# Kernel optimization log

Measured on AMD Instinct MI355X. Metric: run time of the kernel, lower is better.

## Reference

```python
import jax, jax.numpy as jnp
import numpy as np

B, N = 4, 2048
VD, CD = 256, 64
H = 4
INNER = VD  # inner_ratio = 1
D = INNER // H  # head_dim = 64
EPS = 1e-5
RMS_EPS = 1e-6


def layer_norm(x, g, b):
    m = jnp.mean(x, axis=-1, keepdims=True)
    v = jnp.mean((x - m) ** 2, axis=-1, keepdims=True)
    return (x - m) * jax.lax.rsqrt(v + EPS) * g + b


def rms_norm(x, s):
    ms = jnp.mean(x * x, axis=-1, keepdims=True)
    return x * jax.lax.rsqrt(ms + RMS_EPS) * s


def split_heads(x):  # (b, n, h*d) -> (b, h, n, d)
    b, n, _ = x.shape
    return x.reshape(b, n, H, D).transpose(0, 2, 1, 3)


def setup_inputs() -> dict:
    key = jax.random.key(0)
    ks = jax.random.split(key, 10)
    w = lambda k, shp: jax.random.normal(k, shp, dtype=jnp.float32) * 0.02
    return {
        "V": jax.random.normal(ks[0], (B, N, VD), dtype=jnp.float32),
        "C": jax.random.normal(ks[1], (B, N, CD), dtype=jnp.float32),
        "vn_g": jnp.ones((VD,), jnp.float32), "vn_b": jnp.zeros((VD,), jnp.float32),
        "cn_g": jnp.ones((CD,), jnp.float32), "cn_b": jnp.zeros((CD,), jnp.float32),
        "W_vqk": w(ks[2], (VD, 2 * INNER)), "b_vqk": jnp.zeros((2 * INNER,), jnp.float32),
        "rms_v": jnp.ones((2 * INNER,), jnp.float32),
        "W_cqk": w(ks[3], (CD, 2 * INNER)), "b_cqk": jnp.zeros((2 * INNER,), jnp.float32),
        "rms_c": jnp.ones((2 * INNER,), jnp.float32),
        "W_vv": w(ks[4], (VD, INNER)), "b_vv": jnp.zeros((INNER,), jnp.float32),
        "W_cv": w(ks[5], (CD, INNER)), "b_cv": jnp.zeros((INNER,), jnp.float32),
        "W_ov": w(ks[6], (INNER, VD)), "b_ov": jnp.zeros((VD,), jnp.float32),
        "W_oc": w(ks[7], (INNER, CD)), "b_oc": jnp.zeros((CD,), jnp.float32),
    }


def reference(V, C, vn_g, vn_b, cn_g, cn_b, W_vqk, b_vqk, rms_v, W_cqk, b_cqk, rms_c,
              W_vv, b_vv, W_cv, b_cv, W_ov, b_ov, W_oc, b_oc):
    Vn = layer_norm(V, vn_g, vn_b)
    Cn = layer_norm(C, cn_g, cn_b)
    qkv = rms_norm(Vn @ W_vqk + b_vqk, rms_v)
    qkc = rms_norm(Cn @ W_cqk + b_cqk, rms_c)
    qv, kv = jnp.split(qkv, 2, axis=-1)
    qc, kc = jnp.split(qkc, 2, axis=-1)
    vv = Vn @ W_vv + b_vv
    vc = Cn @ W_cv + b_cv
    qv, kv, vv, qc, kc, vc = map(split_heads, (qv, kv, vv, qc, kc, vc))
    # shared attention map: softmax((QvKv^T + QcKc^T)/sqrt(d))
    scores = (jnp.einsum("bhnd,bhmd->bhnm", qv, kv)
              + jnp.einsum("bhnd,bhmd->bhnm", qc, kc)) / np.sqrt(D).astype(np.float32)
    attn = jax.nn.softmax(scores, axis=-1)
    out_v = jnp.einsum("bhnm,bhmd->bhnd", attn, vv).transpose(0, 2, 1, 3).reshape(B, N, INNER)
    out_c = jnp.einsum("bhnm,bhmd->bhnd", attn, vc).transpose(0, 2, 1, 3).reshape(B, N, INNER)
    return out_v @ W_ov + b_ov, out_c @ W_oc + b_oc
```

## Files before the change

kernel.cpp:

```cpp
#include <hip/hip_runtime.h>

typedef unsigned short u16;
typedef unsigned int   u32;
typedef short s16x8 __attribute__((ext_vector_type(8)));
typedef float f32x4 __attribute__((ext_vector_type(4)));

#define WS_STATSV 0
#define WS_STATSC 65536
#define WS_WT_VQK 131072
#define WS_WT_CQK 393216
#define WS_WT_VV  458752
#define WS_WT_CV  589824
#define WS_WT_OV  622592
#define WS_WT_OC  753664
#define WS_Q      786432
#define WS_K      9175040
#define WS_VT     17563648
#define WS_OV     25952256
#define WS_OC     30146560

__device__ __forceinline__ float bf2f(u16 h){
  union { u32 u; float f; } x; x.u = ((u32)h) << 16; return x.f;
}
__device__ __forceinline__ u16 f2bf(float f){
  union { float f; u32 u; } x; x.f = f;
  u32 u = x.u; u += 0x7fffu + ((u >> 16) & 1u);
  return (u16)(u >> 16);
}
__device__ __forceinline__ f32x4 mfma16(s16x8 a, s16x8 b, f32x4 c){
  return __builtin_amdgcn_mfma_f32_16x16x32_bf16(a, b, c, 0, 0, 0);
}

__global__ __launch_bounds__(256) void k_prep(const float* V, const float* C,
    const float* vng, const float* vnb, const float* cng, const float* cnb,
    const float* Wvqk, const float* Wcqk, const float* Wvv, const float* Wcv,
    const float* Wov, const float* Woc, char* ws){
  int bid = blockIdx.x;
  if (bid < 4096){
    int wid = threadIdx.x >> 6, lane = threadIdx.x & 63;
    if (bid < 2048){
      int row = bid*4 + wid;
      const float4* p = (const float4*)(V + row*256);
      float4 v = p[lane];
      float s = v.x+v.y+v.z+v.w, s2 = v.x*v.x+v.y*v.y+v.z*v.z+v.w*v.w;
      for (int d=1; d<64; d<<=1){ s += __shfl_xor(s,d); s2 += __shfl_xor(s2,d); }
      float m = s*(1.0f/256.0f); float var = s2*(1.0f/256.0f) - m*m; if (var < 0.f) var = 0.f;
      float rstd = rsqrtf(var + 1e-5f), nb = -m*rstd;
      float4 gg = ((const float4*)vng)[lane];
      float4 bb = ((const float4*)vnb)[lane];
      ushort4 pk;
      pk.x = f2bf(fmaf(fmaf(v.x, rstd, nb), gg.x, bb.x));
      pk.y = f2bf(fmaf(fmaf(v.y, rstd, nb), gg.y, bb.y));
      pk.z = f2bf(fmaf(fmaf(v.z, rstd, nb), gg.z, bb.z));
      pk.w = f2bf(fmaf(fmaf(v.w, rstd, nb), gg.w, bb.w));
      *(ushort4*)((u16*)(ws + WS_OV) + row*256 + lane*4) = pk;
    } else {
      int row = (bid-2048)*4 + wid;
      float x = C[row*64 + lane];
      float s = x, s2 = x*x;
      for (int d=1; d<64; d<<=1){ s += __shfl_xor(s,d); s2 += __shfl_xor(s2,d); }
      float m = s*(1.0f/64.0f); float var = s2*(1.0f/64.0f) - m*m; if (var < 0.f) var = 0.f;
      float rstd = rsqrtf(var + 1e-5f);
      float xn = fmaf(fmaf(x, rstd, -m*rstd), cng[lane], cnb[lane]);
      ((u16*)(ws + WS_OC))[row*64 + lane] = f2bf(xn);
    }
  } else {
    int tb = bid - 4096;
    const float* src; u16* dst; int K, N, rel;
    if      (tb <  64){ src=Wvqk; dst=(u16*)(ws+WS_WT_VQK); K=256; N=512; rel=tb;     }
    else if (tb <  80){ src=Wcqk; dst=(u16*)(ws+WS_WT_CQK); K=64;  N=512; rel=tb-64;  }
    else if (tb < 112){ src=Wvv;  dst=(u16*)(ws+WS_WT_VV);  K=256; N=256; rel=tb-80;  }
    else if (tb < 120){ src=Wcv;  dst=(u16*)(ws+WS_WT_CV);  K=64;  N=256; rel=tb-112; }
    else if (tb < 152){ src=Wov;  dst=(u16*)(ws+WS_WT_OV);  K=256; N=256; rel=tb-120; }
    else              { src=Woc;  dst=(u16*)(ws+WS_WT_OC);  K=256; N=64;  rel=tb-152; }
    int e = rel*2048 + threadIdx.x*8;
    int k = e / N, n0 = e % N;
    float4 t0 = *(const float4*)(src + e);
    float4 t1 = *(const float4*)(src + e + 4);
    dst[(n0+0)*K + k] = f2bf(t0.x);
    dst[(n0+1)*K + k] = f2bf(t0.y);
    dst[(n0+2)*K + k] = f2bf(t0.z);
    dst[(n0+3)*K + k] = f2bf(t0.w);
    dst[(n0+4)*K + k] = f2bf(t1.x);
    dst[(n0+5)*K + k] = f2bf(t1.y);
    dst[(n0+6)*K + k] = f2bf(t1.z);
    dst[(n0+7)*K + k] = f2bf(t1.w);
  }
}

__global__ __launch_bounds__(256) void k_proj(const float* bvqk, const float* bcqk,
    const float* rmsv, const float* rmsc, const float* bvv, const float* bcv, char* ws){
  __shared__ float ssl[4][16];
  int bid = blockIdx.x;
  int tid = threadIdx.x, lane = tid & 63, w = tid >> 6;
  int c = lane & 15, q = lane >> 4;

  if (bid < 1024){
    bool csd = bid >= 512;
    int rb = (bid & 511) * 16;
    const u16* An    = (const u16*)(ws + (csd ? WS_OC : WS_OV));
    int K            = csd ? 64 : 256;
    const u16* Wt    = (const u16*)(ws + (csd ? WS_WT_CQK : WS_WT_VQK));
    const float* bias= csd ? bcqk : bvqk;
    const float* rms = csd ? rmsc : rmsv;
    int dOff         = csd ? 64 : 0;

    int row = rb + c;
    int j0 = w * 128;

    f32x4 acc[8];
    #pragma unroll
    for (int f=0; f<8; f++){ f32x4 z = {0.f,0.f,0.f,0.f}; acc[f] = z; }

    int nkc = K >> 5;
    for (int kc=0; kc<nkc; kc++){
      int k0 = kc*32 + q*8;
      s16x8 af = *(const s16x8*)(An + row*K + k0);
      #pragma unroll
      for (int f=0; f<8; f++){
        s16x8 bfr = *(const s16x8*)(Wt + (j0 + f*16 + c)*K + k0);
        acc[f] = mfma16(af, bfr, acc[f]);
      }
    }

    float ss[4] = {0.f,0.f,0.f,0.f};
    float rsv[8];
    #pragma unroll
    for (int f=0; f<8; f++){
      int j = j0 + f*16 + c;
      float bsv = bias[j]; rsv[f] = rms[j];
      #pragma unroll
      for (int i=0;i<4;i++){ acc[f][i] += bsv; ss[i] += acc[f][i]*acc[f][i]; }
    }
    #pragma unroll
    for (int d=1; d<16; d<<=1){
      #pragma unroll
      for (int i=0;i<4;i++) ss[i] += __shfl_xor(ss[i], d);
    }
    if (c == 0){
      #pragma unroll
      for (int i=0;i<4;i++) ssl[w][q*4 + i] = ss[i];
    }
    __syncthreads();
    float rmsr[4];
    #pragma unroll
    for (int i=0;i<4;i++){
      int rl = q*4 + i;
      float tot = ssl[0][rl] + ssl[1][rl] + ssl[2][rl] + ssl[3][rl];
      rmsr[i] = rsqrtf(tot * (1.0f/512.0f) + 1e-6f);
    }
    if (w < 2){
      u16* dstb = (u16*)(ws + WS_Q);
      const float qs = 0.125f*1.44269504f;
      #pragma unroll
      for (int f=0; f<8; f++){
        int jj = (j0 + f*16 + c) & 255;
        int head = jj >> 6, dd = (jj & 63) + dOff;
        #pragma unroll
        for (int i=0;i<4;i++){
          int r = rb + q*4 + i;
          int b_ = r >> 11, n = r & 2047;
          dstb[((b_*4 + head)*2048 + n)*128 + dd] = f2bf(acc[f][i]*rmsr[i]*rsv[f]*qs);
        }
      }
    } else {
      u16* kfb = (u16*)(ws + WS_K);
      #pragma unroll
      for (int f=0; f<8; f++){
        int jj = (j0 + f*16 + c) & 255;
        int head = jj >> 6, dd = (jj & 63) + dOff;
        int kcK = dd >> 5, qK = (dd >> 3) & 3, eK = dd & 7;
        #pragma unroll
        for (int i=0;i<4;i++){
          int r = rb + q*4 + i;
          int b_ = r >> 11, n = r & 2047;
          int t = n >> 5, fK = (n >> 4) & 1, cK = n & 15;
          kfb[(b_*4 + head)*262144 + t*4096 + (fK*4 + kcK)*512 + (qK*16 + cK)*8 + eK]
            = f2bf(acc[f][i]*rmsr[i]*rsv[f]);
        }
      }
    }
  } else {
    int vb2 = bid - 1024;
    bool csd = vb2 >= 256;
    int rb = (vb2 & 255) * 32;
    const u16* An    = (const u16*)(ws + (csd ? WS_OC : WS_OV));
    int K            = csd ? 64 : 256;
    const u16* Wt    = (const u16*)(ws + (csd ? WS_WT_CV : WS_WT_VV));
    const float* bias= csd ? bcv : bvv;
    int dOff         = csd ? 64 : 0;

    int s = w & 1, cgp = w >> 1;
    int r0 = rb + s*16, row = r0 + c;
    int j0 = cgp * 128;

    f32x4 acc[8];
    #pragma unroll
    for (int f=0; f<8; f++){ f32x4 z = {0.f,0.f,0.f,0.f}; acc[f] = z; }

    int nkc = K >> 5;
    for (int kc=0; kc<nkc; kc++){
      int k0 = kc*32 + q*8;
      s16x8 af = *(const s16x8*)(An + row*K + k0);
      #pragma unroll
      for (int f=0; f<8; f++){
        s16x8 bfr = *(const s16x8*)(Wt + (j0 + f*16 + c)*K + k0);
        acc[f] = mfma16(af, bfr, acc[f]);
      }
    }
    u16* vfb = (u16*)(ws + WS_VT);
    int r = r0 + q*4;
    int b_ = r >> 11, n = r & 2047;
    int t = n >> 5, m = n & 31;
    int qV = (m < 16) ? (m >> 2) : ((m >> 2) - 4);
    int e0 = (m < 16) ? 0 : 4;
    #pragma unroll
    for (int f=0; f<8; f++){
      int j = j0 + f*16 + c;
      float bv_ = bias[j];
      int head = j >> 6, dd = (j & 63) + dOff;
      int f8 = dd >> 4, cV = dd & 15;
      ushort4 pk;
      pk.x = f2bf(acc[f][0] + bv_); pk.y = f2bf(acc[f][1] + bv_);
      pk.z = f2bf(acc[f][2] + bv_); pk.w = f2bf(acc[f][3] + bv_);
      *(ushort4*)(vfb + (b_*4 + head)*262144 + t*4096 + f8*512 + (qV*16 + cV)*8 + e0) = pk;
    }
  }
}

__global__ __launch_bounds__(256, 2) void k_attn(char* ws){
  const u16* Qw = (const u16*)(ws + WS_Q);
  const u16* KF = (const u16*)(ws + WS_K);
  const u16* VF = (const u16*)(ws + WS_VT);
  u16* Ov = (u16*)(ws + WS_OV);
  u16* Oc = (u16*)(ws + WS_OC);
  __shared__ float mg[2][64][67];

  int bh = blockIdx.x & 15, qb = blockIdx.x >> 4;
  int tid = threadIdx.x, lane = tid & 63, w = tid >> 6;
  int c = lane & 15, q = lane >> 4;
  int g = w & 1, h = w >> 1;
  int qr0 = qb*64 + g*32;

  s16x8 qf[2][4];
  #pragma unroll
  for (int s=0;s<2;s++)
    #pragma unroll
    for (int kc=0;kc<4;kc++)
      qf[s][kc] = *(const s16x8*)(Qw + (bh*2048 + qr0 + s*16 + c)*128 + kc*32 + q*8);

  const u16* kb = KF + bh*262144 + h*131072 + lane*8;
  const u16* vb = VF + bh*262144 + h*131072 + lane*8;

  f32x4 o[2][8];
  float lsum[2] = {0.f, 0.f};
  #pragma unroll
  for (int s=0;s<2;s++)
    #pragma unroll
    for (int f8=0;f8<8;f8++){ f32x4 z = {0.f,0.f,0.f,0.f}; o[s][f8] = z; }

  s16x8 kA[2][4], vA[8], kB[2][4], vB[8];

  auto loadT = [&](s16x8 (&kf)[2][4], s16x8 (&vf)[8], int tt){
    const u16* kt = kb + tt*4096;
    const u16* vt = vb + tt*4096;
    #pragma unroll
    for (int f=0;f<2;f++)
      #pragma unroll
      for (int kc=0;kc<4;kc++)
        kf[f][kc] = *(const s16x8*)(kt + (f*4+kc)*512);
    #pragma unroll
    for (int f8=0;f8<8;f8++)
      vf[f8] = *(const s16x8*)(vt + f8*512);
  };

  auto comp = [&](const s16x8 (&kf)[2][4], const s16x8 (&vf)[8]){
    f32x4 sfr[2][2];
    #pragma unroll
    for (int s=0;s<2;s++)
      #pragma unroll
      for (int f=0;f<2;f++){ f32x4 z = {0.f,0.f,0.f,0.f}; sfr[s][f] = z; }
    #pragma unroll
    for (int s=0;s<2;s++)
      #pragma unroll
      for (int f=0;f<2;f++)
        #pragma unroll
        for (int kc=0;kc<4;kc++)
          sfr[s][f] = mfma16(kf[f][kc], qf[s][kc], sfr[s][f]);

    #pragma unroll
    for (int s=0;s<2;s++){
      float p0 = exp2f(sfr[s][0][0]), p1 = exp2f(sfr[s][0][1]);
      float p2 = exp2f(sfr[s][0][2]), p3 = exp2f(sfr[s][0][3]);
      float p4 = exp2f(sfr[s][1][0]), p5 = exp2f(sfr[s][1][1]);
      float p6 = exp2f(sfr[s][1][2]), p7 = exp2f(sfr[s][1][3]);
      lsum[s] += ((p0+p1)+(p2+p3)) + ((p4+p5)+(p6+p7));
      union { u32 u[4]; s16x8 v; } pa;
      pa.u[0] = (u32)f2bf(p0) | ((u32)f2bf(p1) << 16);
      pa.u[1] = (u32)f2bf(p2) | ((u32)f2bf(p3) << 16);
      pa.u[2] = (u32)f2bf(p4) | ((u32)f2bf(p5) << 16);
      pa.u[3] = (u32)f2bf(p6) | ((u32)f2bf(p7) << 16);
      #pragma unroll
      for (int f8=0;f8<8;f8++)
        o[s][f8] = mfma16(pa.v, vf[f8], o[s][f8]);
    }
  };

  loadT(kA, vA, 0);
  for (int tt=0; tt<32; tt+=2){
    loadT(kB, vB, tt+1);
    comp(kA, vA);
    if (tt+2 < 32) loadT(kA, vA, tt+2);
    comp(kB, vB);
  }

  __syncthreads();
  if (h == 1){
    float* d = &mg[g][lane][0];
    #pragma unroll
    for (int s=0;s<2;s++)
      #pragma unroll
      for (int f8=0;f8<8;f8++)
        #pragma unroll
        for (int i=0;i<4;i++) d[(s*8+f8)*4 + i] = o[s][f8][i];
    d[64] = lsum[0]; d[65] = lsum[1];
  }
  __syncthreads();
  if (h == 0){
    float* d = &mg[g][lane][0];
    #pragma unroll
    for (int s=0;s<2;s++)
      #pragma unroll
      for (int f8=0;f8<8;f8++)
        #pragma unroll
        for (int i=0;i<4;i++) o[s][f8][i] += d[(s*8+f8)*4 + i];
    lsum[0] += d[64]; lsum[1] += d[65];

    #pragma unroll
    for (int s=0;s<2;s++){
      lsum[s] += __shfl_xor(lsum[s], 16);
      lsum[s] += __shfl_xor(lsum[s], 32);
    }

    int b_ = bh >> 2, hh = bh & 3;
    #pragma unroll
    for (int s=0;s<2;s++){
      float inv[4];
      #pragma unroll
      for (int i=0;i<4;i++) inv[i] = 1.0f/__shfl(lsum[s], q*4 + i);
      #pragma unroll
      for (int f8=0;f8<8;f8++){
        int col = f8*16 + c;
        u16* dst = (col < 64) ? Ov : Oc;
        int ddim = col & 63;
        #pragma unroll
        for (int i=0;i<4;i++){
          int n = qr0 + s*16 + q*4 + i;
          dst[(b_*2048 + n)*256 + hh*64 + ddim] = f2bf(o[s][f8][i]*inv[i]);
        }
      }
    }
  }
}

__global__ __launch_bounds__(256) void k_out(const u16* Av, const u16* Wtv, const float* bv,
                                             const u16* Ac, const u16* Wtc, const float* bc,
                                             float* out){
  int bid = blockIdx.x;
  int tid = threadIdx.x, lane = tid & 63, w = tid >> 6;
  int c = lane & 15, q = lane >> 4;
  if (bid < 512){
    int rb = bid * 16;
    int row = rb + c;
    int j0 = w * 64;
    f32x4 acc[4];
    #pragma unroll
    for (int f=0; f<4; f++){ f32x4 z = {0.f,0.f,0.f,0.f}; acc[f] = z; }
    for (int kc=0; kc<8; kc++){
      int k0 = kc*32 + q*8;
      s16x8 af = *(const s16x8*)(Av + row*256 + k0);
      #pragma unroll
      for (int f=0; f<4; f++){
        s16x8 bfr = *(const s16x8*)(Wtv + (j0 + f*16 + c)*256 + k0);
        acc[f] = mfma16(af, bfr, acc[f]);
      }
    }
    #pragma unroll
    for (int f=0; f<4; f++){
      int j = j0 + f*16 + c;
      float bb = bv[j];
      #pragma unroll
      for (int i=0;i<4;i++)
        out[(rb + q*4 + i)*256 + j] = acc[f][i] + bb;
    }
  } else {
    int rb = (bid - 512) * 64;
    int r0 = rb + w*16, row = r0 + c;
    f32x4 acc[4];
    #pragma unroll
    for (int f=0; f<4; f++){ f32x4 z = {0.f,0.f,0.f,0.f}; acc[f] = z; }
    for (int kc=0; kc<8; kc++){
      int k0 = kc*32 + q*8;
      s16x8 af = *(const s16x8*)(Ac + row*256 + k0);
      #pragma unroll
      for (int f=0; f<4; f++){
        s16x8 bfr = *(const s16x8*)(Wtc + (f*16 + c)*256 + k0);
        acc[f] = mfma16(af, bfr, acc[f]);
      }
    }
    float* oc = out + 2097152;
    #pragma unroll
    for (int f=0; f<4; f++){
      int j = f*16 + c;
      float bb = bc[j];
      #pragma unroll
      for (int i=0;i<4;i++)
        oc[(r0 + q*4 + i)*64 + j] = acc[f][i] + bb;
    }
  }
}

extern "C" void kernel_launch(void* const* d_in, const int* in_sizes, int n_in,
                              void* d_out, int out_size, void* d_ws, size_t ws_size,
                              hipStream_t stream){
  (void)in_sizes; (void)n_in; (void)out_size; (void)ws_size;
  const float* V    = (const float*)d_in[0];
  const float* C    = (const float*)d_in[1];
  const float* vng  = (const float*)d_in[2];
  const float* vnb  = (const float*)d_in[3];
  const float* cng  = (const float*)d_in[4];
  const float* cnb  = (const float*)d_in[5];
  const float* Wvqk = (const float*)d_in[6];
  const float* bvqk = (const float*)d_in[7];
  const float* rmsv = (const float*)d_in[8];
  const float* Wcqk = (const float*)d_in[9];
  const float* bcqk = (const float*)d_in[10];
  const float* rmsc = (const float*)d_in[11];
  const float* Wvv  = (const float*)d_in[12];
  const float* bvv  = (const float*)d_in[13];
  const float* Wcv  = (const float*)d_in[14];
  const float* bcv  = (const float*)d_in[15];
  const float* Wov  = (const float*)d_in[16];
  const float* bov  = (const float*)d_in[17];
  const float* Woc  = (const float*)d_in[18];
  const float* boc  = (const float*)d_in[19];
  char* ws = (char*)d_ws;
  float* out = (float*)d_out;

  k_prep<<<4256, 256, 0, stream>>>(V, C, vng, vnb, cng, cnb,
                                   Wvqk, Wcqk, Wvv, Wcv, Wov, Woc, ws);
  k_proj<<<1536, 256, 0, stream>>>(bvqk, bcqk, rmsv, rmsc, bvv, bcv, ws);
  k_attn<<<512, 256, 0, stream>>>(ws);
  k_out<<<640, 256, 0, stream>>>((const u16*)(ws + WS_OV), (const u16*)(ws + WS_WT_OV), bov,
                                 (const u16*)(ws + WS_OC), (const u16*)(ws + WS_WT_OC), boc,
                                 out);
}
```

Measured before the change: 203.3 us.

## Split attention keys four ways per block and double grid size

Each attention block now covers 32 query rows, and its four waves each process a quarter of the key sequence (16 tiles each instead of 32), in place of two query groups with a two-way key split. The grid doubles to 1024 blocks and launch bounds ask for 4 blocks per CU, to raise parallelism and occupancy on the attention kernel. The partial outputs are combined with a two-level LDS tree reduction that adds extra barriers. The higher launch-bound target may also force register spilling given the large accumulator state, and each block now loads its Q fragments for half as many rows, so Q reuse per block drops.

```diff
diff --git a/kernel.cpp b/kernel.cpp
--- a/kernel.cpp
+++ b/kernel.cpp
@@ -228,7 +228,7 @@
   }
 }
 
-__global__ __launch_bounds__(256, 2) void k_attn(char* ws){
+__global__ __launch_bounds__(256, 4) void k_attn(char* ws){
   const u16* Qw = (const u16*)(ws + WS_Q);
   const u16* KF = (const u16*)(ws + WS_K);
   const u16* VF = (const u16*)(ws + WS_VT);
@@ -237,10 +237,9 @@
   __shared__ float mg[2][64][67];
 
   int bh = blockIdx.x & 15, qb = blockIdx.x >> 4;
-  int tid = threadIdx.x, lane = tid & 63, w = tid >> 6;
+  int tid = threadIdx.x, lane = tid & 63, h = tid >> 6;
   int c = lane & 15, q = lane >> 4;
-  int g = w & 1, h = w >> 1;
-  int qr0 = qb*64 + g*32;
+  int qr0 = qb*32;
 
   s16x8 qf[2][4];
   #pragma unroll
@@ -249,8 +248,8 @@
     for (int kc=0;kc<4;kc++)
       qf[s][kc] = *(const s16x8*)(Qw + (bh*2048 + qr0 + s*16 + c)*128 + kc*32 + q*8);
 
-  const u16* kb = KF + bh*262144 + h*131072 + lane*8;
-  const u16* vb = VF + bh*262144 + h*131072 + lane*8;
+  const u16* kb = KF + bh*262144 + h*65536 + lane*8;
+  const u16* vb = VF + bh*262144 + h*65536 + lane*8;
 
   f32x4 o[2][8];
   float lsum[2] = {0.f, 0.f};
@@ -307,16 +306,16 @@
   };
 
   loadT(kA, vA, 0);
-  for (int tt=0; tt<32; tt+=2){
+  for (int tt=0; tt<16; tt+=2){
     loadT(kB, vB, tt+1);
     comp(kA, vA);
-    if (tt+2 < 32) loadT(kA, vA, tt+2);
+    if (tt+2 < 16) loadT(kA, vA, tt+2);
     comp(kB, vB);
   }
 
   __syncthreads();
-  if (h == 1){
-    float* d = &mg[g][lane][0];
+  if (h == 1 || h == 3){
+    float* d = &mg[h>>1][lane][0];
     #pragma unroll
     for (int s=0;s<2;s++)
       #pragma unroll
@@ -326,8 +325,30 @@
     d[64] = lsum[0]; d[65] = lsum[1];
   }
   __syncthreads();
+  if (h == 0 || h == 2){
+    float* d = &mg[h>>1][lane][0];
+    #pragma unroll
+    for (int s=0;s<2;s++)
+      #pragma unroll
+      for (int f8=0;f8<8;f8++)
+        #pragma unroll
+        for (int i=0;i<4;i++) o[s][f8][i] += d[(s*8+f8)*4 + i];
+    lsum[0] += d[64]; lsum[1] += d[65];
+  }
+  __syncthreads();
+  if (h == 2){
+    float* d = &mg[0][lane][0];
+    #pragma unroll
+    for (int s=0;s<2;s++)
+      #pragma unroll
+      for (int f8=0;f8<8;f8++)
+        #pragma unroll
+        for (int i=0;i<4;i++) d[(s*8+f8)*4 + i] = o[s][f8][i];
+    d[64] = lsum[0]; d[65] = lsum[1];
+  }
+  __syncthreads();
   if (h == 0){
-    float* d = &mg[g][lane][0];
+    float* d = &mg[0][lane][0];
     #pragma unroll
     for (int s=0;s<2;s++)
       #pragma unroll
@@ -450,7 +471,7 @@
   k_prep<<<4256, 256, 0, stream>>>(V, C, vng, vnb, cng, cnb,
                                    Wvqk, Wcqk, Wvv, Wcv, Wov, Woc, ws);
   k_proj<<<1536, 256, 0, stream>>>(bvqk, bcqk, rmsv, rmsc, bvv, bcv, ws);
-  k_attn<<<512, 256, 0, stream>>>(ws);
+  k_attn<<<1024, 256, 0, stream>>>(ws);
   k_out<<<640, 256, 0, stream>>>((const u16*)(ws + WS_OV), (const u16*)(ws + WS_WT_OV), bov,
                                  (const u16*)(ws + WS_OC), (const u16*)(ws + WS_WT_OC), boc,
                                  out);
```

Result: slower. 655.4 us (+222.4%).
